# Performance work log

Measured on AMD Instinct MI355X. Metric: run time of the kernel, lower is better.

The kernel has to match this reference:

```python
import jax, jax.numpy as jnp
import numpy as np

B, D, F, K = 2048, 2048, 32768, 64  # batch, activation_dim, dict_size, top-k


def setup_inputs() -> dict:
    key = jax.random.key(0)
    k1, k2, k3 = jax.random.split(key, 3)
    x = jax.random.normal(k1, (B, D), dtype=jnp.float32)
    # tied-ish init: encoder/decoder drawn independently here (values don't affect math)
    W_enc = jax.random.normal(k2, (F, D), dtype=jnp.float32) * 0.02
    W_dec = jax.random.normal(k3, (D, F), dtype=jnp.float32) * 0.02
    b_enc = jnp.zeros((F,), dtype=jnp.float32)
    b_dec = jnp.zeros((D,), dtype=jnp.float32)
    return {"x": x, "W_enc": W_enc, "b_enc": b_enc, "W_dec": W_dec, "b_dec": b_dec, "k": K}


def reference(x, W_enc, b_enc, W_dec, b_dec, k):
    # Encode: mu = x @ W_enc^T + b_enc  (var_flag=0 so z = mu)
    mu = jnp.einsum("bd,fd->bf", x, W_enc) + b_enc  # [B, F]
    # Abs top-k selection
    _, top_idx = jax.lax.top_k(jnp.abs(mu), k)              # [B, K]
    selected_vals = jnp.take_along_axis(mu, top_idx, axis=-1)  # [B, K] signed values
    # Scatter into dense sparse_features
    rows = jnp.arange(mu.shape[0])[:, None]                 # [B, 1]
    sparse_features = jnp.zeros_like(mu).at[rows, top_idx].set(selected_vals)
    # Decode (april update mode: decoder has bias)
    x_hat = jnp.einsum("bf,df->bd", sparse_features, W_dec) + b_dec  # [B, D]
    return x_hat
```

## Files before the change

### kernel.cpp

```cpp
#include <hip/hip_runtime.h>
#include <stdint.h>

#define B_ROWS 2048
#define DIM    2048
#define FDICT  32768
#define KSEL   64
#define TOPC   96
#define CAP    1536
#define THRFAC 2.35f
#define WSAMPN (64 * DIM)

typedef __attribute__((ext_vector_type(8))) short bf16x8;
typedef __attribute__((ext_vector_type(4))) float f32x4;

__device__ __forceinline__ float bf16_to_f32(ushort u)
{
    return __uint_as_float(((uint32_t)u) << 16);
}

__global__ __launch_bounds__(256) void zero_kernel(int* __restrict__ cand_cnt,
                                                   float* __restrict__ wsum)
{
    int i = blockIdx.x * 256 + threadIdx.x;
    if (i < B_ROWS) cand_cnt[i] = 0;
    if (i == 0) wsum[0] = 0.f;
}

__global__ __launch_bounds__(256) void wstat_kernel(
    const float* __restrict__ Wenc, float* __restrict__ wsum)
{
    __shared__ float red[256];
    const int tid = threadIdx.x;
    float s = 0.f;
    for (int i = blockIdx.x * 256 + tid; i < WSAMPN / 4; i += 8 * 256) {
        float4 w = ((const float4*)Wenc)[i];
        s += w.x * w.x + w.y * w.y + w.z * w.z + w.w * w.w;
    }
    red[tid] = s;
    __syncthreads();
    for (int o = 128; o > 0; o >>= 1) {
        if (tid < o) red[tid] += red[tid + o];
        __syncthreads();
    }
    if (tid == 0) atomicAdd(wsum, red[0]);
}

__global__ __launch_bounds__(256) void rownorm_kernel(
    const float* __restrict__ x, const float* __restrict__ wsum,
    float* __restrict__ T)
{
    __shared__ float red[256];
    const int row = blockIdx.x;
    const int tid = threadIdx.x;
    const float4* xr = (const float4*)(x + (size_t)row * DIM);
    float s = 0.f;
#pragma unroll
    for (int u = 0; u < 2; ++u) {
        float4 v = xr[tid + u * 256];
        s += v.x * v.x + v.y * v.y + v.z * v.z + v.w * v.w;
    }
    red[tid] = s;
    __syncthreads();
    for (int o = 128; o > 0; o >>= 1) {
        if (tid < o) red[tid] += red[tid + o];
        __syncthreads();
    }
    if (tid == 0)
        T[row] = THRFAC * sqrtf(wsum[0] / (float)WSAMPN) * sqrtf(red[0]);
}

__global__ __launch_bounds__(256) void conv_bf16_kernel(
    const float* __restrict__ src, ushort* __restrict__ dst)
{
    const size_t i = ((size_t)blockIdx.x * 256 + threadIdx.x) * 8;
    float4 u = *(const float4*)(src + i);
    float4 v = *(const float4*)(src + i + 4);
    union { ushort s[8]; bf16x8 w; } o;
    float t[8] = {u.x, u.y, u.z, u.w, v.x, v.y, v.z, v.w};
#pragma unroll
    for (int j = 0; j < 8; ++j) {
        union { __bf16 h; ushort s; } cv;
        cv.h = (__bf16)t[j];
        o.s[j] = cv.s;
    }
    *(bf16x8*)(dst + i) = o.w;
}

#define GM 128
#define GN 128
#define GK 32
#define NT (DIM / GK)

__device__ __forceinline__ void gload_lds16(const void* g, void* l)
{
    __builtin_amdgcn_global_load_lds(
        (const __attribute__((address_space(1))) void*)(uintptr_t)g,
        (__attribute__((address_space(3))) void*)(uint32_t)(uintptr_t)l,
        16, 0, 0);
}

__global__ __launch_bounds__(256) void enc_gemm_cand(
    const ushort* __restrict__ A,
    const ushort* __restrict__ Bw,
    const float* __restrict__ benc,
    const float* __restrict__ T,
    float* __restrict__ cand_val,
    int* __restrict__ cand_idx,
    int* __restrict__ cand_cnt)
{
    __shared__ __align__(16) ushort As[2][GM * GK];
    __shared__ __align__(16) ushort Bs[2][GN * GK];

    const int tid  = threadIdx.x;
    const int lane = tid & 63;
    const int wv   = tid >> 6;
    const int wr   = wv >> 1, wc = wv & 1;
    const int lr   = lane & 15, lg = lane >> 4;

    const int bid = blockIdx.x;
    const int nf  = (bid & 7) * 512 + (bid >> 3);
    const int row0 = (nf & 15) * GM;
    const int col0 = (nf >> 4) * GN;

    const ushort* aSrc = A  + (size_t)row0 * DIM;
    const ushort* bSrc = Bw + (size_t)col0 * DIM;

    f32x4 acc[4][4] = {};

#define STAGE(bsel, kt)                                                        \
    {                                                                          \
        const int k0_ = (kt) * GK;                                             \
        _Pragma("unroll")                                                      \
        for (int i_ = 0; i_ < 2; ++i_) {                                       \
            const int q0_ = wv * 128 + i_ * 64;                                \
            const int q_  = q0_ + lane;                                        \
            const int r_  = q_ >> 2;                                           \
            const int sb_ = (q_ & 3) ^ ((r_ >> 1) & 3);                        \
            gload_lds16(aSrc + (size_t)r_ * DIM + k0_ + sb_ * 8,               \
                        (char*)&As[bsel][0] + q0_ * 16);                       \
            gload_lds16(bSrc + (size_t)r_ * DIM + k0_ + sb_ * 8,               \
                        (char*)&Bs[bsel][0] + q0_ * 16);                       \
        }                                                                      \
    }

    STAGE(0, 0);
    int cur = 0;
    for (int kt = 0; kt < NT; ++kt) {
        __builtin_amdgcn_s_barrier();
        if (kt + 1 < NT) {
            STAGE(cur ^ 1, kt + 1);
            asm volatile("s_waitcnt vmcnt(4)" ::: "memory");
        } else {
            asm volatile("s_waitcnt vmcnt(0)" ::: "memory");
        }
        __builtin_amdgcn_s_barrier();
        __builtin_amdgcn_sched_barrier(0);

        bf16x8 af[4], bfr[4];
#pragma unroll
        for (int mi = 0; mi < 4; ++mi) {
            const int R = wr * 64 + mi * 16 + lr;
            af[mi] = *(const bf16x8*)(&As[cur][0] + R * GK + ((lg ^ ((R >> 1) & 3)) * 8));
        }
#pragma unroll
        for (int ni = 0; ni < 4; ++ni) {
            const int R = wc * 64 + ni * 16 + lr;
            bfr[ni] = *(const bf16x8*)(&Bs[cur][0] + R * GK + ((lg ^ ((R >> 1) & 3)) * 8));
        }
#pragma unroll
        for (int mi = 0; mi < 4; ++mi)
#pragma unroll
            for (int ni = 0; ni < 4; ++ni)
                acc[mi][ni] = __builtin_amdgcn_mfma_f32_16x16x32_bf16(
                    af[mi], bfr[ni], acc[mi][ni], 0, 0, 0);
        cur ^= 1;
    }

    float bias[4];
#pragma unroll
    for (int ni = 0; ni < 4; ++ni)
        bias[ni] = benc[col0 + wc * 64 + ni * 16 + lr];

#pragma unroll
    for (int mi = 0; mi < 4; ++mi) {
#pragma unroll
        for (int r = 0; r < 4; ++r) {
            const int rloc = wr * 64 + mi * 16 + lg * 4 + r;
            const float t = T[row0 + rloc];
#pragma unroll
            for (int ni = 0; ni < 4; ++ni) {
                const float v = acc[mi][ni][r] + bias[ni];
                if (fabsf(v) >= t) {
                    const int grow = row0 + rloc;
                    const int gcol = col0 + wc * 64 + ni * 16 + lr;
                    int pos = atomicAdd(&cand_cnt[grow], 1);
                    if (pos < CAP) {
                        cand_val[(size_t)grow * CAP + pos] = v;
                        cand_idx[(size_t)grow * CAP + pos] = gcol;
                    }
                }
            }
        }
    }
#undef STAGE
}

__global__ __launch_bounds__(256) void select_kernel(
    const float* __restrict__ cand_val,
    const int* __restrict__ cand_idx,
    const int* __restrict__ cand_cnt,
    int* __restrict__ run_idx)
{
    const int row = blockIdx.x;
    const int tid = threadIdx.x;

    __shared__ uint32_t ua[CAP];
    __shared__ int      si[CAP];
    __shared__ int      hist[256];
    __shared__ uint32_t sh_prefix;
    __shared__ int      sh_cgt, c_out, c_eq;

    int cnt = cand_cnt[row];
    if (cnt > CAP) cnt = CAP;

    for (int j = tid; j < cnt; j += 256) {
        ua[j] = __float_as_uint(cand_val[(size_t)row * CAP + j]) & 0x7fffffffu;
        si[j] = cand_idx[(size_t)row * CAP + j];
    }
    if (tid == 0) { sh_prefix = 0u; sh_cgt = 0; c_out = 0; c_eq = 0; }
    __syncthreads();

    if (cnt <= TOPC) {
        if (tid < TOPC) run_idx[(size_t)row * TOPC + tid] = (tid < cnt) ? si[tid] : -1;
        return;
    }

    for (int p = 3; p >= 0; --p) {
        hist[tid] = 0;
        __syncthreads();
        const uint32_t mask = (p == 3) ? 0u : (0xffffffffu << ((p + 1) * 8));
        const uint32_t pref = sh_prefix;
        for (int j = tid; j < cnt; j += 256) {
            uint32_t u = ua[j];
            if ((u & mask) == pref)
                atomicAdd(&hist[(u >> (p * 8)) & 255], 1);
        }
        __syncthreads();
        if (tid == 0) {
            int cum = sh_cgt;
            int chosen = 0;
            for (int b = 255; b >= 0; --b) {
                int c = hist[b];
                if (cum + c >= TOPC) { chosen = b; break; }
                cum += c;
            }
            sh_prefix = sh_prefix | ((uint32_t)chosen << (p * 8));
            sh_cgt = cum;
        }
        __syncthreads();
    }

    const uint32_t uth = sh_prefix;
    for (int j = tid; j < cnt; j += 256) {
        if (ua[j] > uth) {
            int pos = atomicAdd(&c_out, 1);
            run_idx[(size_t)row * TOPC + pos] = si[j];
        }
    }
    __syncthreads();
    const int base = c_out;
    for (int j = tid; j < cnt; j += 256) {
        if (ua[j] == uth) {
            int e = atomicAdd(&c_eq, 1);
            int slot = base + e;
            if (slot < TOPC) run_idx[(size_t)row * TOPC + slot] = si[j];
        }
    }
}

__global__ __launch_bounds__(256) void refine_np_kernel(
    const float* __restrict__ x,
    const float* __restrict__ Wenc,
    const float* __restrict__ benc,
    const int* __restrict__ run_idx,
    float* __restrict__ sel_val,
    int* __restrict__ sel_idx)
{
    const int half = threadIdx.x >> 7;
    const int cid  = threadIdx.x & 127;
    const int row  = blockIdx.x * 2 + half;

    __shared__ __align__(16) float xs[2][DIM];
    __shared__ float cval[2][TOPC];
    __shared__ int   cidx[2][TOPC];

    {
        const float4* src = (const float4*)(x + (size_t)blockIdx.x * 2 * DIM);
        for (int i = threadIdx.x; i < 2 * DIM / 4; i += 256)
            ((float4*)xs)[i] = src[i];
    }
    if (cid < TOPC) cidx[half][cid] = run_idx[(size_t)row * TOPC + cid];
    __syncthreads();

    if (cid < TOPC) {
        const int f = cidx[half][cid];
        if (f >= 0) {
            const float4* w4 = (const float4*)(Wenc + (size_t)f * DIM);
            const float4* x4 = (const float4*)xs[half];
            float a0 = 0.f, a1 = 0.f, a2 = 0.f, a3 = 0.f;
            float4 pa[8], pb[8];
#pragma unroll
            for (int u = 0; u < 8; ++u) pa[u] = w4[u];
            for (int t0 = 0; t0 < DIM / 4; t0 += 16) {
#pragma unroll
                for (int u = 0; u < 8; ++u) pb[u] = w4[t0 + 8 + u];
#pragma unroll
                for (int u = 0; u < 8; ++u) {
                    float4 xv = x4[t0 + u];
                    a0 = __fadd_rn(a0, __fmul_rn(xv.x, pa[u].x));
                    a1 = __fadd_rn(a1, __fmul_rn(xv.y, pa[u].y));
                    a2 = __fadd_rn(a2, __fmul_rn(xv.z, pa[u].z));
                    a3 = __fadd_rn(a3, __fmul_rn(xv.w, pa[u].w));
                }
                if (t0 + 16 < DIM / 4) {
#pragma unroll
                    for (int u = 0; u < 8; ++u) pa[u] = w4[t0 + 16 + u];
                }
#pragma unroll
                for (int u = 0; u < 8; ++u) {
                    float4 xv = x4[t0 + 8 + u];
                    a0 = __fadd_rn(a0, __fmul_rn(xv.x, pb[u].x));
                    a1 = __fadd_rn(a1, __fmul_rn(xv.y, pb[u].y));
                    a2 = __fadd_rn(a2, __fmul_rn(xv.z, pb[u].z));
                    a3 = __fadd_rn(a3, __fmul_rn(xv.w, pb[u].w));
                }
            }
            float v = __fadd_rn(__fadd_rn(a0, a2), __fadd_rn(a1, a3));
            cval[half][cid] = __fadd_rn(v, benc[f]);
        } else {
            cval[half][cid] = 0.f;
        }
    }
    __syncthreads();

    if (cid < TOPC) {
        const int f = cidx[half][cid];
        if (f >= 0) {
            const uint32_t av = __float_as_uint(cval[half][cid]) & 0x7fffffffu;
            int rank = 0;
            for (int u = 0; u < TOPC; ++u) {
                if (u == cid) continue;
                int fu = cidx[half][u];
                if (fu < 0) continue;
                uint32_t au = __float_as_uint(cval[half][u]) & 0x7fffffffu;
                if (au > av || (au == av && fu < f)) ++rank;
            }
            if (rank < KSEL) {
                sel_val[(size_t)row * KSEL + rank] = cval[half][cid];
                sel_idx[(size_t)row * KSEL + rank] = f;
            }
        }
    }
}

__global__ __launch_bounds__(256) void transpose_wdec_bf16(
    const float* __restrict__ Wdec,
    ushort* __restrict__ WdecT)
{
    __shared__ float t[64][65];
    const int f0 = blockIdx.x * 64;
    const int d0 = blockIdx.y * 64;
    const int tx = threadIdx.x & 63;
    const int ty = threadIdx.x >> 6;
#pragma unroll
    for (int r = 0; r < 16; ++r)
        t[ty * 16 + r][tx] = Wdec[(size_t)(d0 + ty * 16 + r) * FDICT + f0 + tx];
    __syncthreads();
#pragma unroll
    for (int r = 0; r < 16; ++r) {
        union { __bf16 h; ushort s; } cv;
        cv.h = (__bf16)t[tx][ty * 16 + r];
        WdecT[(size_t)(f0 + ty * 16 + r) * DIM + d0 + tx] = cv.s;
    }
}

__global__ __launch_bounds__(256) void decode_full_kernel(
    const ushort* __restrict__ WdecT,
    const float* __restrict__ sel_val,
    const int* __restrict__ sel_idx,
    const float* __restrict__ bdec,
    float* __restrict__ out)
{
    const int row = blockIdx.x;
    const int tid = threadIdx.x;
    __shared__ float vv[KSEL];
    __shared__ int   ff[KSEL];
    if (tid < KSEL) {
        vv[tid] = sel_val[row * KSEL + tid];
        ff[tid] = sel_idx[row * KSEL + tid];
    }
    __syncthreads();
    const int d0 = tid * 8;
    float acc[8];
    {
        float4 b0 = *(const float4*)(bdec + d0);
        float4 b1 = *(const float4*)(bdec + d0 + 4);
        acc[0] = b0.x; acc[1] = b0.y; acc[2] = b0.z; acc[3] = b0.w;
        acc[4] = b1.x; acc[5] = b1.y; acc[6] = b1.z; acc[7] = b1.w;
    }
    for (int k = 0; k < KSEL; ++k) {
        const float v = vv[k];
        union { ushort s[8]; bf16x8 w; } u;
        u.w = *(const bf16x8*)(WdecT + (size_t)ff[k] * DIM + d0);
#pragma unroll
        for (int j = 0; j < 8; ++j)
            acc[j] = fmaf(v, bf16_to_f32(u.s[j]), acc[j]);
    }
    float* orow = out + (size_t)row * DIM + d0;
    float4 o0 = {acc[0], acc[1], acc[2], acc[3]};
    float4 o1 = {acc[4], acc[5], acc[6], acc[7]};
    *(float4*)(orow + 0) = o0;
    *(float4*)(orow + 4) = o1;
}

extern "C" void kernel_launch(void* const* d_in, const int* in_sizes, int n_in,
                              void* d_out, int out_size, void* d_ws, size_t ws_size,
                              hipStream_t stream)
{
    const float* x    = (const float*)d_in[0];
    const float* Wenc = (const float*)d_in[1];
    const float* benc = (const float*)d_in[2];
    const float* Wdec = (const float*)d_in[3];
    const float* bdec = (const float*)d_in[4];
    (void)in_sizes; (void)n_in; (void)out_size; (void)ws_size;
    float* out = (float*)d_out;

    char* ws = (char*)d_ws;
    size_t off = 0;
    float*  cand_val = (float*)(ws + off);  off += (size_t)B_ROWS * CAP * 4;
    int*    cand_idx = (int*)(ws + off);    off += (size_t)B_ROWS * CAP * 4;
    int*    cand_cnt = (int*)(ws + off);    off += (size_t)B_ROWS * 4;
    float*  Tthr     = (float*)(ws + off);  off += (size_t)B_ROWS * 4;
    float*  wsum     = (float*)(ws + off);  off += 256;
    ushort* x_bf16   = (ushort*)(ws + off); off += (size_t)B_ROWS * DIM * 2;
    int*    run_idx  = (int*)(ws + off);    off += (size_t)B_ROWS * TOPC * 4;
    float*  sel_val  = (float*)(ws + off);  off += (size_t)B_ROWS * KSEL * 4;
    int*    sel_idx  = (int*)(ws + off);    off += (size_t)B_ROWS * KSEL * 4;
    char*   big      = ws + off;

    zero_kernel<<<(B_ROWS + 255) / 256, 256, 0, stream>>>(cand_cnt, wsum);
    wstat_kernel<<<8, 256, 0, stream>>>(Wenc, wsum);
    rownorm_kernel<<<B_ROWS, 256, 0, stream>>>(x, wsum, Tthr);
    conv_bf16_kernel<<<(B_ROWS * DIM) / (256 * 8), 256, 0, stream>>>(x, x_bf16);

    ushort* wenc_bf = (ushort*)big;
    conv_bf16_kernel<<<(int)(((size_t)FDICT * DIM) / (256 * 8)), 256, 0, stream>>>(
        Wenc, wenc_bf);
    enc_gemm_cand<<<(B_ROWS / GM) * (FDICT / GN), 256, 0, stream>>>(
        x_bf16, wenc_bf, benc, Tthr, cand_val, cand_idx, cand_cnt);

    select_kernel<<<B_ROWS, 256, 0, stream>>>(cand_val, cand_idx, cand_cnt, run_idx);
    refine_np_kernel<<<B_ROWS / 2, 256, 0, stream>>>(x, Wenc, benc, run_idx, sel_val, sel_idx);

    ushort* WdecT = (ushort*)big;
    transpose_wdec_bf16<<<dim3(FDICT / 64, DIM / 64), 256, 0, stream>>>(Wdec, WdecT);
    decode_full_kernel<<<B_ROWS, 256, 0, stream>>>(WdecT, sel_val, sel_idx, bdec, out);
}
```

Measured before the change: 980.6 us.

## Enlarge encoder GEMM tile to 256x256 with 4-slot LDS pipeline and split-phase MFMA

The encoder GEMM moves from 128x128 tiles with 256 threads and double buffering to 256x256 tiles with 512 threads, a four-slot LDS ring prefetching two K-steps ahead, and each iteration split into two MFMA halves interleaved with A/B staging and s_setprio. The aim is more reuse of each loaded tile, fewer blocks, and better overlap of global-to-LDS loads with MFMA work. In exchange it roughly doubles accumulator registers (acc[4][8]), uses far more LDS, and adds barriers per iteration, which may limit occupancy.

```diff
diff --git a/kernel.cpp b/kernel.cpp
--- a/kernel.cpp
+++ b/kernel.cpp
@@ -86,10 +86,11 @@
     *(bf16x8*)(dst + i) = o.w;
 }
 
-#define GM 128
-#define GN 128
+#define GM 256
+#define GN 256
 #define GK 32
-#define NT (DIM / GK)
+#define NHS (DIM / GK)
+#define SLOT (GM * GK)
 
 __device__ __forceinline__ void gload_lds16(const void* g, void* l)
 {
@@ -99,7 +100,7 @@
         16, 0, 0);
 }
 
-__global__ __launch_bounds__(256) void enc_gemm_cand(
+__global__ __launch_bounds__(512, 2) void enc_gemm_cand(
     const ushort* __restrict__ A,
     const ushort* __restrict__ Bw,
     const float* __restrict__ benc,
@@ -108,8 +109,8 @@
     int* __restrict__ cand_idx,
     int* __restrict__ cand_cnt)
 {
-    __shared__ __align__(16) ushort As[2][GM * GK];
-    __shared__ __align__(16) ushort Bs[2][GN * GK];
+    __shared__ __align__(16) ushort As[4][SLOT];
+    __shared__ __align__(16) ushort Bs[4][SLOT];
 
     const int tid  = threadIdx.x;
     const int lane = tid & 63;
@@ -118,68 +119,104 @@
     const int lr   = lane & 15, lg = lane >> 4;
 
     const int bid = blockIdx.x;
-    const int nf  = (bid & 7) * 512 + (bid >> 3);
-    const int row0 = (nf & 15) * GM;
-    const int col0 = (nf >> 4) * GN;
+    const int nf  = (bid & 7) * 128 + (bid >> 3);
+    const int row0 = (nf & 7) * GM;
+    const int col0 = (nf >> 3) * GN;
 
     const ushort* aSrc = A  + (size_t)row0 * DIM;
     const ushort* bSrc = Bw + (size_t)col0 * DIM;
 
-    f32x4 acc[4][4] = {};
-
-#define STAGE(bsel, kt)                                                        \
+    f32x4 acc[4][8] = {};
+
+#define STAGE_A(s_, hs_)                                                       \
     {                                                                          \
-        const int k0_ = (kt) * GK;                                             \
+        const int k0_ = (hs_) * GK;                                            \
         _Pragma("unroll")                                                      \
         for (int i_ = 0; i_ < 2; ++i_) {                                       \
-            const int q0_ = wv * 128 + i_ * 64;                                \
-            const int q_  = q0_ + lane;                                        \
-            const int r_  = q_ >> 2;                                           \
+            const int q_ = tid + i_ * 512;                                     \
+            const int r_ = q_ >> 2;                                            \
             const int sb_ = (q_ & 3) ^ ((r_ >> 1) & 3);                        \
             gload_lds16(aSrc + (size_t)r_ * DIM + k0_ + sb_ * 8,               \
-                        (char*)&As[bsel][0] + q0_ * 16);                       \
+                        (char*)&As[s_][0] + q_ * 16);                          \
+        }                                                                      \
+    }
+#define STAGE_B(s_, hs_)                                                       \
+    {                                                                          \
+        const int k0_ = (hs_) * GK;                                            \
+        _Pragma("unroll")                                                      \
+        for (int i_ = 0; i_ < 2; ++i_) {                                       \
+            const int q_ = tid + i_ * 512;                                     \
+            const int r_ = q_ >> 2;                                            \
+            const int sb_ = (q_ & 3) ^ ((r_ >> 1) & 3);                        \
             gload_lds16(bSrc + (size_t)r_ * DIM + k0_ + sb_ * 8,               \
-                        (char*)&Bs[bsel][0] + q0_ * 16);                       \
+                        (char*)&Bs[s_][0] + q_ * 16);                          \
         }                                                                      \
     }
-
-    STAGE(0, 0);
-    int cur = 0;
-    for (int kt = 0; kt < NT; ++kt) {
+#define LDSF(Mat, s_, R_) \
+    (*(const bf16x8*)(&Mat[s_][0] + (R_) * GK + ((lg ^ (((R_) >> 1) & 3)) << 3)))
+
+    STAGE_A(0, 0); STAGE_B(0, 0);
+    STAGE_A(1, 1); STAGE_B(1, 1);
+    asm volatile("s_waitcnt vmcnt(4)" ::: "memory");
+    __builtin_amdgcn_s_barrier();
+    __builtin_amdgcn_sched_barrier(0);
+
+    for (int hs = 0; hs < NHS; ++hs) {
+        const int s = hs & 3;
+        bf16x8 af[4], bf0[4];
+#pragma unroll
+        for (int mi = 0; mi < 4; ++mi) {
+            const int R = wr * 64 + mi * 16 + lr;
+            af[mi] = LDSF(As, s, R);
+        }
+#pragma unroll
+        for (int ni = 0; ni < 4; ++ni) {
+            const int R = wc * 128 + ni * 16 + lr;
+            bf0[ni] = LDSF(Bs, s, R);
+        }
+        if (hs + 2 < NHS) STAGE_A((hs + 2) & 3, hs + 2);
         __builtin_amdgcn_s_barrier();
-        if (kt + 1 < NT) {
-            STAGE(cur ^ 1, kt + 1);
+        __builtin_amdgcn_sched_barrier(0);
+        __builtin_amdgcn_s_setprio(1);
+#pragma unroll
+        for (int mi = 0; mi < 4; ++mi)
+#pragma unroll
+            for (int ni = 0; ni < 4; ++ni)
+                acc[mi][ni] = __builtin_amdgcn_mfma_f32_16x16x32_bf16(
+                    af[mi], bf0[ni], acc[mi][ni], 0, 0, 0);
+        __builtin_amdgcn_s_setprio(0);
+        __builtin_amdgcn_s_barrier();
+        __builtin_amdgcn_sched_barrier(0);
+        bf16x8 bf1[4];
+#pragma unroll
+        for (int ni = 0; ni < 4; ++ni) {
+            const int R = wc * 128 + (ni + 4) * 16 + lr;
+            bf1[ni] = LDSF(Bs, s, R);
+        }
+        if (hs + 2 < NHS) {
+            STAGE_B((hs + 2) & 3, hs + 2);
             asm volatile("s_waitcnt vmcnt(4)" ::: "memory");
         } else {
             asm volatile("s_waitcnt vmcnt(0)" ::: "memory");
         }
         __builtin_amdgcn_s_barrier();
         __builtin_amdgcn_sched_barrier(0);
-
-        bf16x8 af[4], bfr[4];
-#pragma unroll
-        for (int mi = 0; mi < 4; ++mi) {
-            const int R = wr * 64 + mi * 16 + lr;
-            af[mi] = *(const bf16x8*)(&As[cur][0] + R * GK + ((lg ^ ((R >> 1) & 3)) * 8));
-        }
-#pragma unroll
-        for (int ni = 0; ni < 4; ++ni) {
-            const int R = wc * 64 + ni * 16 + lr;
-            bfr[ni] = *(const bf16x8*)(&Bs[cur][0] + R * GK + ((lg ^ ((R >> 1) & 3)) * 8));
-        }
+        __builtin_amdgcn_s_setprio(1);
 #pragma unroll
         for (int mi = 0; mi < 4; ++mi)
 #pragma unroll
             for (int ni = 0; ni < 4; ++ni)
-                acc[mi][ni] = __builtin_amdgcn_mfma_f32_16x16x32_bf16(
-                    af[mi], bfr[ni], acc[mi][ni], 0, 0, 0);
-        cur ^= 1;
-    }
-
-    float bias[4];
-#pragma unroll
-    for (int ni = 0; ni < 4; ++ni)
-        bias[ni] = benc[col0 + wc * 64 + ni * 16 + lr];
+                acc[mi][ni + 4] = __builtin_amdgcn_mfma_f32_16x16x32_bf16(
+                    af[mi], bf1[ni], acc[mi][ni + 4], 0, 0, 0);
+        __builtin_amdgcn_s_setprio(0);
+        __builtin_amdgcn_s_barrier();
+        __builtin_amdgcn_sched_barrier(0);
+    }
+
+    float bias[8];
+#pragma unroll
+    for (int ni = 0; ni < 8; ++ni)
+        bias[ni] = benc[col0 + wc * 128 + ni * 16 + lr];
 
 #pragma unroll
     for (int mi = 0; mi < 4; ++mi) {
@@ -188,11 +225,11 @@
             const int rloc = wr * 64 + mi * 16 + lg * 4 + r;
             const float t = T[row0 + rloc];
 #pragma unroll
-            for (int ni = 0; ni < 4; ++ni) {
+            for (int ni = 0; ni < 8; ++ni) {
                 const float v = acc[mi][ni][r] + bias[ni];
                 if (fabsf(v) >= t) {
                     const int grow = row0 + rloc;
-                    const int gcol = col0 + wc * 64 + ni * 16 + lr;
+                    const int gcol = col0 + wc * 128 + ni * 16 + lr;
                     int pos = atomicAdd(&cand_cnt[grow], 1);
                     if (pos < CAP) {
                         cand_val[(size_t)grow * CAP + pos] = v;
@@ -202,7 +239,9 @@
             }
         }
     }
-#undef STAGE
+#undef STAGE_A
+#undef STAGE_B
+#undef LDSF
 }
 
 __global__ __launch_bounds__(256) void select_kernel(
@@ -456,7 +495,7 @@
     ushort* wenc_bf = (ushort*)big;
     conv_bf16_kernel<<<(int)(((size_t)FDICT * DIM) / (256 * 8)), 256, 0, stream>>>(
         Wenc, wenc_bf);
-    enc_gemm_cand<<<(B_ROWS / GM) * (FDICT / GN), 256, 0, stream>>>(
+    enc_gemm_cand<<<(B_ROWS / GM) * (FDICT / GN), 512, 0, stream>>>(
         x_bf16, wenc_bf, benc, Tthr, cand_val, cand_idx, cand_cnt);
 
     select_kernel<<<B_ROWS, 256, 0, stream>>>(cand_val, cand_idx, cand_cnt, run_idx);
```

Result: faster. 958.5 us (-2.3%).
